# Performance work log

Hardware: AMD Instinct MI355X
Metric: run time of the kernel (lower is better)

## Reference

```python
import jax, jax.numpy as jnp
import numpy as np

D_MODEL, D_STATE, D_CONV, EXPAND = 1024, 16, 4, 2
D_INNER = EXPAND * D_MODEL            # 2048
DT_RANK = -(-D_MODEL // 16)           # ceil(d_model/16) = 64
B_SZ, L_SEQ = 2, 2048


def setup_inputs() -> dict:
    key = jax.random.key(0)
    ks = jax.random.split(key, 8)
    s = 0.02
    x = jax.random.normal(ks[0], (B_SZ, L_SEQ, D_MODEL), dtype=jnp.float32)
    W_in = jax.random.normal(ks[1], (D_MODEL, 2 * D_INNER), dtype=jnp.float32) * s
    conv_w = jax.random.normal(ks[2], (D_INNER, 1, D_CONV), dtype=jnp.float32) * 0.1  # depthwise (O,I/g,K)
    conv_b = jnp.zeros((D_INNER,), dtype=jnp.float32)
    W_x = jax.random.normal(ks[3], (D_INNER, DT_RANK + 2 * D_STATE), dtype=jnp.float32) * s
    W_dt = jax.random.normal(ks[4], (DT_RANK, D_INNER), dtype=jnp.float32) * s
    b_dt = jax.random.normal(ks[5], (D_INNER,), dtype=jnp.float32) * 0.1
    A_log = jnp.log(jnp.tile(jnp.arange(1, D_STATE + 1, dtype=jnp.float32), (D_INNER, 1)))  # (d_in, n)
    D_param = jnp.ones((D_INNER,), dtype=jnp.float32)
    W_out = jax.random.normal(ks[6], (D_INNER, D_MODEL), dtype=jnp.float32) * s
    return {"x": x, "W_in": W_in, "conv_w": conv_w, "conv_b": conv_b,
            "W_x": W_x, "W_dt": W_dt, "b_dt": b_dt, "A_log": A_log,
            "D_param": D_param, "W_out": W_out}


def _mamba(x, W_in, conv_w, conv_b, W_x, W_dt, b_dt, A_log, D_param, W_out):
    b, l, _ = x.shape
    d_in, n = A_log.shape
    dt_rank = W_dt.shape[0]
    d_conv = conv_w.shape[-1]

    xr = x @ W_in                                  # (b, l, 2*d_in)
    xs, res = xr[..., :d_in], xr[..., d_in:]

    # causal depthwise conv1d (left pad d_conv-1, truncate to l)
    xc = jnp.transpose(xs, (0, 2, 1))              # (b, d_in, l)
    xc = jax.lax.conv_general_dilated(
        xc, conv_w, window_strides=(1,), padding=[(d_conv - 1, 0)],
        dimension_numbers=("NCH", "OIH", "NCH"), feature_group_count=d_in)
    xc = xc + conv_b[None, :, None]
    xc = jnp.transpose(xc, (0, 2, 1))              # (b, l, d_in)
    xc = jax.nn.silu(xc)

    # SSM parameterization
    x_dbl = xc @ W_x                               # (b, l, dt_rank + 2n)
    delta = jax.nn.softplus(x_dbl[..., :dt_rank] @ W_dt + b_dt)   # (b, l, d_in)
    Bm = x_dbl[..., dt_rank:dt_rank + n]           # (b, l, n)
    Cm = x_dbl[..., dt_rank + n:]                  # (b, l, n)
    A = -jnp.exp(A_log)                            # (d_in, n)

    deltaA = jnp.exp(jnp.einsum("bld,dn->bldn", delta, A))        # (b, l, d_in, n)
    dBu = jnp.einsum("bld,bld,bln->bldn", delta, xc, Bm)          # (b, l, d_in, n)

    def step(h, inp):
        dA_t, dBu_t, C_t = inp                     # (b,d,n), (b,d,n), (b,n)
        h = dA_t * h + dBu_t
        y_t = jnp.einsum("bdn,bn->bd", h, C_t)
        return h, y_t

    h0 = jnp.zeros((b, d_in, n), dtype=xc.dtype)
    _, ys = jax.lax.scan(
        step, h0,
        (jnp.transpose(deltaA, (1, 0, 2, 3)),
         jnp.transpose(dBu, (1, 0, 2, 3)),
         jnp.transpose(Cm, (1, 0, 2))))
    y = jnp.transpose(ys, (1, 0, 2)) + xc * D_param  # (b, l, d_in)

    y = y * jax.nn.silu(res)
    return y @ W_out                               # (b, l, d_model)


def reference(x, W_in, conv_w, conv_b, W_x, W_dt, b_dt, A_log, D_param, W_out):
    return _mamba(x, W_in, conv_w, conv_b, W_x, W_dt, b_dt, A_log, D_param, W_out)
```

## Files before the change

### kernel.cpp

```cpp
#include <hip/hip_runtime.h>
#include <math.h>

#define B_SZ    2
#define L_SEQ   2048
#define D_MODEL 1024
#define D_INNER 2048
#define D_STATE 16
#define DT_RANK 64
#define MM      (B_SZ * L_SEQ)
#define NCH     64
#define CLEN    (L_SEQ / NCH)
#define PFD     8

typedef _Float16 h8v __attribute__((ext_vector_type(8)));
typedef _Float16 h4v __attribute__((ext_vector_type(4)));
typedef float f32x4 __attribute__((ext_vector_type(4)));

__device__ __forceinline__ void gload16(const void* g, void* l) {
    __builtin_amdgcn_global_load_lds((const __attribute__((address_space(1))) void*)g,
                                     (__attribute__((address_space(3))) void*)l, 16, 0, 0);
}

__global__ __launch_bounds__(256) void prep(const float* __restrict__ x,
                                            _Float16* __restrict__ xf16,
                                            const float* __restrict__ W_in,
                                            _Float16* __restrict__ WinT,
                                            const float* __restrict__ W_x,
                                            _Float16* __restrict__ WxT,
                                            const float* __restrict__ W_dt,
                                            _Float16* __restrict__ WdtT,
                                            const float* __restrict__ W_out,
                                            _Float16* __restrict__ WoutT,
                                            const float* __restrict__ cw,
                                            float* __restrict__ cwT) {
    __shared__ float t[32][33];
    const int b = blockIdx.x;
    const float* W; _Float16* T; int K, N, tile;
    if (b < 4096)      { W = W_in;  T = WinT;  K = 1024; N = 4096; tile = b; }
    else if (b < 4288) { W = W_x;   T = WxT;   K = 2048; N = 96;   tile = b - 4096; }
    else if (b < 4416) { W = W_dt;  T = WdtT;  K = 64;   N = 2048; tile = b - 4288; }
    else if (b < 6464) { W = W_out; T = WoutT; K = 2048; N = 1024; tile = b - 4416; }
    else if (b < 10560) {
        int idx = (b - 6464) * 256 + threadIdx.x;
        float4 v = ((const float4*)x)[idx];
        h4v h = {(_Float16)v.x, (_Float16)v.y, (_Float16)v.z, (_Float16)v.w};
        *(h4v*)(xf16 + (size_t)idx * 4) = h;
        return;
    } else {
        for (int i = threadIdx.x; i < D_INNER * 4; i += 256) {
            int d = i >> 2, k = i & 3;
            cwT[k * D_INNER + d] = cw[i];
        }
        return;
    }
    const int ntx = N / 32;
    const int k0 = (tile / ntx) * 32, n0 = (tile % ntx) * 32;
    #pragma unroll
    for (int i = 0; i < 4; ++i) {
        int idx = threadIdx.x + i * 256;
        int r = idx >> 5, c = idx & 31;
        t[r][c] = W[(size_t)(k0 + r) * N + n0 + c];
    }
    __syncthreads();
    #pragma unroll
    for (int i = 0; i < 4; ++i) {
        int idx = threadIdx.x + i * 256;
        int n = idx >> 5, k = idx & 31;
        T[(size_t)(n0 + n) * K + k0 + k] = (_Float16)t[k][n];
    }
}

template<int EPI>
__global__ __launch_bounds__(256) void gemm_f16(const _Float16* __restrict__ A,
                                                const _Float16* __restrict__ Bt,
                                                const float* __restrict__ bias,
                                                float* __restrict__ C,
                                                _Float16* __restrict__ H,
                                                _Float16* __restrict__ Hg,
                                                int M, int N, int K, int ldc) {
    __shared__ _Float16 smemh[16384];

    const int tid = threadIdx.x;
    const int wave = tid >> 6, lane = tid & 63;
    const int bm = blockIdx.y * 128, bn = blockIdx.x * 128;

    const int lrow = lane >> 2, pc = lane & 3;
    const int ar = wave * 32 + lrow;
    const size_t gA = (size_t)(bm + ar) * K + ((pc ^ ((ar >> 1) & 3)) * 8);
    const size_t gB = (size_t)(bn + ar) * K + ((pc ^ ((ar >> 1) & 3)) * 8);
    const int lofs = (wave * 32) * 32;

    const int lm = lane & 15, lq = lane >> 4;
    const int rofs = (lq ^ ((lm >> 1) & 3)) * 8;
    const int wm = (wave >> 1) * 64, wn = (wave & 1) * 64;

    f32x4 acc[4][4];
    #pragma unroll
    for (int i = 0; i < 4; ++i)
        #pragma unroll
        for (int j = 0; j < 4; ++j) acc[i][j] = (f32x4){0.f, 0.f, 0.f, 0.f};

    gload16(A + gA, smemh + lofs);
    gload16(A + gA + (size_t)16 * K, smemh + lofs + 16 * 32);
    gload16(Bt + gB, smemh + 8192 + lofs);
    gload16(Bt + gB + (size_t)16 * K, smemh + 8192 + lofs + 16 * 32);
    __syncthreads();

    int kb = 0;
    for (int k0 = 0; k0 < K; k0 += 32, kb ^= 1) {
        if (k0 + 32 < K) {
            int nb = kb ^ 1;
            gload16(A + gA + k0 + 32, smemh + nb * 4096 + lofs);
            gload16(A + gA + k0 + 32 + (size_t)16 * K, smemh + nb * 4096 + lofs + 16 * 32);
            gload16(Bt + gB + k0 + 32, smemh + 8192 + nb * 4096 + lofs);
            gload16(Bt + gB + k0 + 32 + (size_t)16 * K, smemh + 8192 + nb * 4096 + lofs + 16 * 32);
        }

        const _Float16* sA = smemh + kb * 4096;
        const _Float16* sB = smemh + 8192 + kb * 4096;
        h8v fa[4], fb[4];
        #pragma unroll
        for (int i = 0; i < 4; ++i) {
            fa[i] = *(const h8v*)&sA[(wm + i * 16 + lm) * 32 + rofs];
            fb[i] = *(const h8v*)&sB[(wn + i * 16 + lm) * 32 + rofs];
        }
        #pragma unroll
        for (int mi = 0; mi < 4; ++mi)
            #pragma unroll
            for (int ni = 0; ni < 4; ++ni)
                acc[mi][ni] = __builtin_amdgcn_mfma_f32_16x16x32_f16(fa[mi], fb[ni], acc[mi][ni], 0, 0, 0);
        __syncthreads();
    }

    if (EPI == 0) {
        float* ep = (float*)smemh + wave * 1088;
        #pragma unroll
        for (int mi = 0; mi < 4; ++mi) {
            #pragma unroll
            for (int ni = 0; ni < 4; ++ni)
                #pragma unroll
                for (int r = 0; r < 4; ++r)
                    ep[(lq * 4 + r) * 68 + ni * 16 + lm] = acc[mi][ni][r];
            int rowb = bm + wm + mi * 16;
            #pragma unroll
            for (int i = 0; i < 4; ++i) {
                int ch = lane + 64 * i;
                int row = ch >> 4, c4 = (ch & 15) * 4;
                *(float4*)&C[(size_t)(rowb + row) * ldc + bn + wn + c4] =
                    *(const float4*)&ep[row * 68 + c4];
            }
        }
    } else {
        _Float16* ep = smemh + wave * 1152;
        const bool gate = (EPI == 2) && (bn >= 2048);
        _Float16* dst = gate ? Hg : H;
        const int cb = bn + wn - (gate ? 2048 : 0);
        #pragma unroll
        for (int mi = 0; mi < 4; ++mi) {
            #pragma unroll
            for (int ni = 0; ni < 4; ++ni) {
                int col = bn + wn + ni * 16 + lm;
                #pragma unroll
                for (int r = 0; r < 4; ++r) {
                    float v = acc[mi][ni][r];
                    if (EPI == 1) {
                        float a = v + bias[col];
                        v = (a > 20.f) ? a : log1pf(__expf(a));
                    } else if (gate) {
                        v = v / (1.f + __expf(-v));
                    }
                    ep[(lq * 4 + r) * 72 + ni * 16 + lm] = (_Float16)v;
                }
            }
            int rowb = bm + wm + mi * 16;
            #pragma unroll
            for (int i = 0; i < 2; ++i) {
                int ch = lane + 64 * i;
                int row = ch >> 3, c8 = (ch & 7) * 8;
                *(h8v*)&dst[(size_t)(rowb + row) * ldc + cb + c8] =
                    *(const h8v*)&ep[row * 72 + c8];
            }
        }
    }
}

__global__ __launch_bounds__(256) void gemm_xd(const _Float16* __restrict__ xch,
                                               const _Float16* __restrict__ WxT,
                                               _Float16* __restrict__ xdh,
                                               float* __restrict__ Bm,
                                               float* __restrict__ Cm) {
    __shared__ _Float16 sA[64 * 32];
    __shared__ _Float16 sB[96 * 32];
    const int tid = threadIdx.x;
    const int m0 = blockIdx.x * 64;
    const int wave = tid >> 6, lane = tid & 63;
    const int lm = lane & 15, lq = lane >> 4;
    const int rofs = (lq ^ ((lm >> 1) & 3)) * 8;

    const int wr = tid >> 2, wc = tid & 3, c0 = wc * 8;
    const int wofsA = wr * 32 + ((wc ^ ((wr >> 1) & 3)) * 8);
    const int wr2 = 64 + wr;
    const int wofsB2 = wr2 * 32 + ((wc ^ ((wr2 >> 1) & 3)) * 8);

    f32x4 acc[6];
    #pragma unroll
    for (int i = 0; i < 6; ++i) acc[i] = (f32x4){0.f, 0.f, 0.f, 0.f};

    h8v pA = *(const h8v*)(xch + (size_t)(m0 + wr) * D_INNER + c0);
    h8v pB0 = *(const h8v*)(WxT + (size_t)wr * D_INNER + c0);
    h8v pB1 = (tid < 128) ? *(const h8v*)(WxT + (size_t)wr2 * D_INNER + c0) : (h8v)0;

    for (int k0 = 0; k0 < D_INNER; k0 += 32) {
        *(h8v*)&sA[wofsA] = pA;
        *(h8v*)&sB[wofsA] = pB0;
        if (tid < 128) *(h8v*)&sB[wofsB2] = pB1;
        __syncthreads();

        if (k0 + 32 < D_INNER) {
            int kk = k0 + 32 + c0;
            pA = *(const h8v*)(xch + (size_t)(m0 + wr) * D_INNER + kk);
            pB0 = *(const h8v*)(WxT + (size_t)wr * D_INNER + kk);
            if (tid < 128) pB1 = *(const h8v*)(WxT + (size_t)wr2 * D_INNER + kk);
        }

        h8v fa = *(const h8v*)&sA[(wave * 16 + lm) * 32 + rofs];
        #pragma unroll
        for (int nf = 0; nf < 6; ++nf) {
            h8v fb = *(const h8v*)&sB[(nf * 16 + lm) * 32 + rofs];
            acc[nf] = __builtin_amdgcn_mfma_f32_16x16x32_f16(fa, fb, acc[nf], 0, 0, 0);
        }
        __syncthreads();
    }

    #pragma unroll
    for (int nf = 0; nf < 6; ++nf) {
        int col = nf * 16 + lm;
        #pragma unroll
        for (int r = 0; r < 4; ++r) {
            int row = m0 + wave * 16 + lq * 4 + r;
            float v = acc[nf][r];
            if (col < 64)      xdh[(size_t)row * 64 + col] = (_Float16)v;
            else if (col < 80) Bm[(size_t)row * 16 + (col - 64)] = v;
            else               Cm[(size_t)row * 16 + (col - 80)] = v;
        }
    }
}

__global__ __launch_bounds__(256) void conv_silu(const _Float16* __restrict__ xsh,
                                                 const float* __restrict__ cwT,
                                                 const float* __restrict__ cb,
                                                 _Float16* __restrict__ xch) {
    int idx = blockIdx.x * 256 + threadIdx.x;
    int d0 = (idx * 8) & (D_INNER - 1);
    int m  = (idx * 8) >> 11;
    int l  = m & (L_SEQ - 1);
    float acc[8];
    {
        float4 c0 = *(const float4*)&cb[d0];
        float4 c1 = *(const float4*)&cb[d0 + 4];
        acc[0] = c0.x; acc[1] = c0.y; acc[2] = c0.z; acc[3] = c0.w;
        acc[4] = c1.x; acc[5] = c1.y; acc[6] = c1.z; acc[7] = c1.w;
    }
    #pragma unroll
    for (int k = 0; k < 4; ++k) {
        int ll = l - 3 + k;
        if (ll >= 0) {
            h8v v = *(const h8v*)(xsh + (size_t)(m - 3 + k) * D_INNER + d0);
            float4 w0 = *(const float4*)&cwT[k * D_INNER + d0];
            float4 w1 = *(const float4*)&cwT[k * D_INNER + d0 + 4];
            acc[0] += (float)v[0] * w0.x; acc[1] += (float)v[1] * w0.y;
            acc[2] += (float)v[2] * w0.z; acc[3] += (float)v[3] * w0.w;
            acc[4] += (float)v[4] * w1.x; acc[5] += (float)v[5] * w1.y;
            acc[6] += (float)v[6] * w1.z; acc[7] += (float)v[7] * w1.w;
        }
    }
    h8v o;
    #pragma unroll
    for (int j = 0; j < 8; ++j) {
        float s = acc[j] / (1.f + __expf(-acc[j]));
        o[j] = (_Float16)s;
    }
    *(h8v*)(xch + (size_t)idx * 8) = o;
}

__global__ __launch_bounds__(256) void scan_part1(const _Float16* __restrict__ deltah,
                                                  const _Float16* __restrict__ xch,
                                                  const float* __restrict__ Bm,
                                                  const float* __restrict__ A_log,
                                                  float* __restrict__ hlocal,
                                                  float* __restrict__ Ssum) {
    const int t = threadIdx.x;
    const int d = blockIdx.x * 256 + t;
    const int c = blockIdx.y;
    const int b = blockIdx.z;

    float An[16];
    {
        const float4* ap = (const float4*)(A_log + (size_t)d * 16);
        #pragma unroll
        for (int q = 0; q < 4; ++q) {
            float4 v = ap[q];
            An[q * 4 + 0] = -__expf(v.x); An[q * 4 + 1] = -__expf(v.y);
            An[q * 4 + 2] = -__expf(v.z); An[q * 4 + 3] = -__expf(v.w);
        }
    }
    const float An0 = An[0];
    bool fast = An0 < 0.f;
    #pragma unroll
    for (int n = 0; n < 16; ++n)
        fast = fast && (fabsf(An[n] - (float)(n + 1) * An0) < 1e-3f * fabsf(An[n]));

    __shared__ float sB[CLEN][16];
    {
        size_t l0 = (size_t)(b * L_SEQ + c * CLEN) * 16;
        #pragma unroll
        for (int i = 0; i < (CLEN * 16) / 256; ++i) {
            int idx = t + i * 256;
            sB[idx >> 4][idx & 15] = Bm[l0 + idx];
        }
    }
    __syncthreads();

    float h[16];
    #pragma unroll
    for (int n = 0; n < 16; ++n) h[n] = 0.f;
    float S = 0.f;

    size_t base = (size_t)(b * L_SEQ + c * CLEN) * D_INNER + d;
    float bd[PFD], bx[PFD];
    #pragma unroll
    for (int i = 0; i < PFD; ++i) {
        bd[i] = (float)deltah[base + (size_t)i * D_INNER];
        bx[i] = (float)xch[base + (size_t)i * D_INNER];
    }

    if (fast) {
        for (int jb = 0; jb < CLEN; jb += PFD) {
            #pragma unroll
            for (int i = 0; i < PFD; ++i) {
                int j = jb + i;
                float dv = bd[i], xv = bx[i];
                int jn = j + PFD;
                if (jn < CLEN) {
                    bd[i] = (float)deltah[base + (size_t)jn * D_INNER];
                    bx[i] = (float)xch[base + (size_t)jn * D_INNER];
                }
                S += dv;
                float dbx = dv * xv;
                float r = __expf(dv * An0);
                float pw = r;
                #pragma unroll
                for (int n = 0; n < 16; ++n) {
                    h[n] = pw * h[n] + dbx * sB[j][n];
                    pw *= r;
                }
            }
        }
    } else {
        for (int jb = 0; jb < CLEN; jb += PFD) {
            #pragma unroll
            for (int i = 0; i < PFD; ++i) {
                int j = jb + i;
                float dv = bd[i], xv = bx[i];
                int jn = j + PFD;
                if (jn < CLEN) {
                    bd[i] = (float)deltah[base + (size_t)jn * D_INNER];
                    bx[i] = (float)xch[base + (size_t)jn * D_INNER];
                }
                S += dv;
                float dbx = dv * xv;
                #pragma unroll
                for (int n = 0; n < 16; ++n)
                    h[n] = __expf(dv * An[n]) * h[n] + dbx * sB[j][n];
            }
        }
    }

    size_t o = ((size_t)(b * NCH + c) * D_INNER + d) * 16;
    float4* hp = (float4*)(hlocal + o);
    #pragma unroll
    for (int q = 0; q < 4; ++q)
        hp[q] = make_float4(h[q * 4], h[q * 4 + 1], h[q * 4 + 2], h[q * 4 + 3]);
    Ssum[(size_t)(b * NCH + c) * D_INNER + d] = S;
}

__global__ __launch_bounds__(256) void scan_combine(const float* __restrict__ hlocal,
                                                    const float* __restrict__ Ssum,
                                                    const float* __restrict__ A_log,
                                                    float* __restrict__ h0buf) {
    int gid = blockIdx.x * 256 + threadIdx.x;
    int n = gid & 15;
    int d = (gid >> 4) & (D_INNER - 1);
    int b = gid >> 15;
    float An = -__expf(A_log[(size_t)d * 16 + n]);
    float H = 0.f;
    float pS[4], pH[4];
    #pragma unroll
    for (int i = 0; i < 4; ++i) {
        size_t sc = (size_t)(b * NCH + i) * D_INNER + d;
        pS[i] = Ssum[sc];
        pH[i] = hlocal[sc * 16 + n];
    }
    for (int cb = 0; cb < NCH; cb += 4) {
        #pragma unroll
        for (int i = 0; i < 4; ++i) {
            int c = cb + i;
            float S = pS[i], hl = pH[i];
            int cn = c + 4;
            if (cn < NCH) {
                size_t sc = (size_t)(b * NCH + cn) * D_INNER + d;
                pS[i] = Ssum[sc];
                pH[i] = hlocal[sc * 16 + n];
            }
            size_t o = ((size_t)(b * NCH + c) * D_INNER + d) * 16 + n;
            h0buf[o] = H;
            H = __expf(An * S) * H + hl;
        }
    }
}

__global__ __launch_bounds__(256) void scan_part2(const _Float16* __restrict__ deltah,
                                                  const _Float16* __restrict__ xch,
                                                  const float* __restrict__ Bm,
                                                  const float* __restrict__ Cm,
                                                  const float* __restrict__ h0buf,
                                                  const float* __restrict__ A_log,
                                                  const float* __restrict__ Dp,
                                                  const _Float16* __restrict__ sresh,
                                                  _Float16* __restrict__ yhalf) {
    const int t = threadIdx.x;
    const int d = blockIdx.x * 256 + t;
    const int c = blockIdx.y;
    const int b = blockIdx.z;

    float An[16];
    {
        const float4* ap = (const float4*)(A_log + (size_t)d * 16);
        #pragma unroll
        for (int q = 0; q < 4; ++q) {
            float4 v = ap[q];
            An[q * 4 + 0] = -__expf(v.x); An[q * 4 + 1] = -__expf(v.y);
            An[q * 4 + 2] = -__expf(v.z); An[q * 4 + 3] = -__expf(v.w);
        }
    }
    const float An0 = An[0];
    bool fast = An0 < 0.f;
    #pragma unroll
    for (int n = 0; n < 16; ++n)
        fast = fast && (fabsf(An[n] - (float)(n + 1) * An0) < 1e-3f * fabsf(An[n]));

    __shared__ float sB[CLEN][16];
    __shared__ float sC[CLEN][16];
    {
        size_t l0 = (size_t)(b * L_SEQ + c * CLEN) * 16;
        #pragma unroll
        for (int i = 0; i < (CLEN * 16) / 256; ++i) {
            int idx = t + i * 256;
            sB[idx >> 4][idx & 15] = Bm[l0 + idx];
            sC[idx >> 4][idx & 15] = Cm[l0 + idx];
        }
    }
    __syncthreads();

    float h[16];
    {
        size_t o = ((size_t)(b * NCH + c) * D_INNER + d) * 16;
        const float4* hp = (const float4*)(h0buf + o);
        #pragma unroll
        for (int q = 0; q < 4; ++q) {
            float4 v = hp[q];
            h[q * 4 + 0] = v.x; h[q * 4 + 1] = v.y;
            h[q * 4 + 2] = v.z; h[q * 4 + 3] = v.w;
        }
    }
    const float Dv = Dp[d];

    size_t base = (size_t)(b * L_SEQ + c * CLEN) * D_INNER + d;
    float bd[PFD], bx[PFD], bg[PFD];
    #pragma unroll
    for (int i = 0; i < PFD; ++i) {
        bd[i] = (float)deltah[base + (size_t)i * D_INNER];
        bx[i] = (float)xch[base + (size_t)i * D_INNER];
        bg[i] = (float)sresh[base + (size_t)i * D_INNER];
    }

    if (fast) {
        for (int jb = 0; jb < CLEN; jb += PFD) {
            #pragma unroll
            for (int i = 0; i < PFD; ++i) {
                int j = jb + i;
                float dv = bd[i], xv = bx[i], gv = bg[i];
                int jn = j + PFD;
                if (jn < CLEN) {
                    bd[i] = (float)deltah[base + (size_t)jn * D_INNER];
                    bx[i] = (float)xch[base + (size_t)jn * D_INNER];
                    bg[i] = (float)sresh[base + (size_t)jn * D_INNER];
                }
                float dbx = dv * xv;
                float r = __expf(dv * An0);
                float pw = r;
                float y = 0.f;
                #pragma unroll
                for (int n = 0; n < 16; ++n) {
                    h[n] = pw * h[n] + dbx * sB[j][n];
                    y += h[n] * sC[j][n];
                    pw *= r;
                }
                float yv = (y + xv * Dv) * gv;
                yhalf[base + (size_t)j * D_INNER] = (_Float16)yv;
            }
        }
    } else {
        for (int jb = 0; jb < CLEN; jb += PFD) {
            #pragma unroll
            for (int i = 0; i < PFD; ++i) {
                int j = jb + i;
                float dv = bd[i], xv = bx[i], gv = bg[i];
                int jn = j + PFD;
                if (jn < CLEN) {
                    bd[i] = (float)deltah[base + (size_t)jn * D_INNER];
                    bx[i] = (float)xch[base + (size_t)jn * D_INNER];
                    bg[i] = (float)sresh[base + (size_t)jn * D_INNER];
                }
                float dbx = dv * xv;
                float y = 0.f;
                #pragma unroll
                for (int n = 0; n < 16; ++n) {
                    h[n] = __expf(dv * An[n]) * h[n] + dbx * sB[j][n];
                    y += h[n] * sC[j][n];
                }
                float yv = (y + xv * Dv) * gv;
                yhalf[base + (size_t)j * D_INNER] = (_Float16)yv;
            }
        }
    }
}

extern "C" void kernel_launch(void* const* d_in, const int* in_sizes, int n_in,
                              void* d_out, int out_size, void* d_ws, size_t ws_size,
                              hipStream_t stream) {
    const float* x      = (const float*)d_in[0];
    const float* W_in   = (const float*)d_in[1];
    const float* conv_w = (const float*)d_in[2];
    const float* conv_b = (const float*)d_in[3];
    const float* W_x    = (const float*)d_in[4];
    const float* W_dt   = (const float*)d_in[5];
    const float* b_dt   = (const float*)d_in[6];
    const float* A_log  = (const float*)d_in[7];
    const float* D_par  = (const float*)d_in[8];
    const float* W_out  = (const float*)d_in[9];
    float* out = (float*)d_out;

    char* wsb = (char*)d_ws;
    _Float16*  xsh    = (_Float16*)(wsb + 0);
    _Float16*  sresh  = (_Float16*)(wsb + 16777216);
    _Float16*  deltah = (_Float16*)(wsb + 33554432);
    _Float16*  xch    = (_Float16*)(wsb + 50331648);
    _Float16*  xf16   = (_Float16*)(wsb + 67108864);
    _Float16*  WinT   = (_Float16*)(wsb + 75497472);
    _Float16*  yhalf  = (_Float16*)(wsb + 67108864);
    _Float16*  WxT    = (_Float16*)(wsb + 83886080);
    _Float16*  WdtT   = (_Float16*)(wsb + 84279296);
    _Float16*  xdh    = (_Float16*)(wsb + 84541440);
    float*     Bbuf   = (float*)(wsb + 85065728);
    float*     Cbuf   = (float*)(wsb + 85327872);
    float*     Ssum   = (float*)(wsb + 85590016);
    float*     hloc   = (float*)(wsb + 86638592);
    float*     h0buf  = (float*)(wsb + 103415808);
    _Float16*  WoutT  = (_Float16*)(wsb + 120193024);
    float*     cwT    = (float*)(wsb + 124387328);

    dim3 blk(256);

    prep<<<dim3(10561), blk, 0, stream>>>(x, xf16, W_in, WinT, W_x, WxT,
                                          W_dt, WdtT, W_out, WoutT, conv_w, cwT);
    gemm_f16<2><<<dim3(32, 32), blk, 0, stream>>>(
        xf16, WinT, nullptr, nullptr, xsh, sresh, MM, 2 * D_INNER, D_MODEL, 2048);
    conv_silu<<<dim3((size_t)MM * D_INNER / 8 / 256), blk, 0, stream>>>(xsh, cwT, conv_b, xch);
    gemm_xd<<<dim3(MM / 64), blk, 0, stream>>>(xch, WxT, xdh, Bbuf, Cbuf);
    gemm_f16<1><<<dim3(16, 32), blk, 0, stream>>>(
        xdh, WdtT, b_dt, nullptr, deltah, nullptr, MM, D_INNER, DT_RANK, D_INNER);
    scan_part1<<<dim3(D_INNER / 256, NCH, B_SZ), blk, 0, stream>>>(deltah, xch, Bbuf, A_log, hloc, Ssum);
    scan_combine<<<dim3(B_SZ * D_INNER * 16 / 256), blk, 0, stream>>>(hloc, Ssum, A_log, h0buf);
    scan_part2<<<dim3(D_INNER / 256, NCH, B_SZ), blk, 0, stream>>>(deltah, xch, Bbuf, Cbuf, h0buf, A_log, D_par, sresh, yhalf);
    gemm_f16<0><<<dim3(8, 32), blk, 0, stream>>>(
        yhalf, WoutT, nullptr, out, nullptr, nullptr, MM, D_MODEL, D_INNER, D_MODEL);
}
```

Measured before the change: 323.5 us.

## Replace input projection GEMM with 256x256-tile 8-wave pipelined MFMA kernel

Adds a dedicated in-projection GEMM kernel using 256x256 output tiles, 512 threads, and double-buffered LDS with global_load_lds prefetch. The prefetch is interleaved with four MFMA phases under setprio and barriers. The goal is more operand reuse per LDS load and better overlap of memory with compute for the largest GEMM. The tradeoff is only 256 blocks on a large-CU GPU, so the grid may fill the machine unevenly, plus heavy register and LDS use at 128KB of shared memory.

Result: faster. 316.4 us (-2.2%).

```diff
diff --git a/kernel.cpp b/kernel.cpp
--- a/kernel.cpp
+++ b/kernel.cpp
@@ -70,6 +70,140 @@
     }
 }
 
+#define LDA_(mi, ks) (*(const h8v*)(smb + cb_ + rowA + (mi) * 2048 + ((ks) ? ps1 : ps0)))
+#define LDB_(ni, ks) (*(const h8v*)(smb + cb_ + 32768 + rowB + (ni) * 2048 + ((ks) ? ps1 : ps0)))
+#define PH(m0, m1) \
+    _Pragma("unroll") \
+    for (int ni = 0; ni < 4; ++ni) { \
+        acc[m0][ni] = __builtin_amdgcn_mfma_f32_16x16x32_f16(aF0, bF[2 * ni],     acc[m0][ni], 0, 0, 0); \
+        acc[m0][ni] = __builtin_amdgcn_mfma_f32_16x16x32_f16(aF1, bF[2 * ni + 1], acc[m0][ni], 0, 0, 0); \
+        acc[m1][ni] = __builtin_amdgcn_mfma_f32_16x16x32_f16(aF2, bF[2 * ni],     acc[m1][ni], 0, 0, 0); \
+        acc[m1][ni] = __builtin_amdgcn_mfma_f32_16x16x32_f16(aF3, bF[2 * ni + 1], acc[m1][ni], 0, 0, 0); \
+    }
+
+__global__ __launch_bounds__(512, 2) void gemm_k1(const _Float16* __restrict__ A,
+                                                  const _Float16* __restrict__ Bt,
+                                                  _Float16* __restrict__ H,
+                                                  _Float16* __restrict__ Hg) {
+    __shared__ _Float16 smem[65536];
+    char* smb = (char*)smem;
+
+    const int tid  = threadIdx.x;
+    const int wave = tid >> 6, lane = tid & 63;
+    const int wm = wave >> 2, wn = wave & 3;
+    const int lm = lane & 15, lq = lane >> 4;
+    const int bm = blockIdx.y * 256, bn = blockIdx.x * 256;
+
+    const int ps0 = ((lq)     ^ (lm & 7)) << 4;
+    const int ps1 = ((lq + 4) ^ (lm & 7)) << 4;
+    const int rowA = (wm * 128 + lm) << 7;
+    const int rowB = (wn * 64 + lm) << 7;
+
+    const int srow  = lane >> 3;
+    const int sslot = (lane & 7) ^ srow;
+    const _Float16* pA = A  + (size_t)(bm + wave * 32 + srow) * 1024 + sslot * 8;
+    const _Float16* pB = Bt + (size_t)(bn + wave * 32 + srow) * 1024 + sslot * 8;
+    char* dA = smb + wave * 4096;
+    char* dB = smb + 32768 + wave * 4096;
+
+    f32x4 acc[8][4];
+    #pragma unroll
+    for (int i = 0; i < 8; ++i)
+        #pragma unroll
+        for (int j = 0; j < 4; ++j) acc[i][j] = (f32x4){0.f, 0.f, 0.f, 0.f};
+
+    #pragma unroll
+    for (int q = 0; q < 4; ++q) {
+        gload16(pA + q * 8192, dA + q * 1024);
+        gload16(pB + q * 8192, dB + q * 1024);
+    }
+    asm volatile("s_waitcnt vmcnt(0)" ::: "memory");
+    __builtin_amdgcn_s_barrier();
+
+    int cb_ = 0;
+    for (int t = 0; t < 16; ++t) {
+        const int nb_ = 65536 - cb_;
+        const bool pf = (t < 15);
+        const size_t kn = (size_t)(t + 1) * 64;
+
+        h8v aF0, aF1, aF2, aF3;
+        h8v bF[8];
+
+        aF0 = LDA_(0, 0); aF1 = LDA_(0, 1); aF2 = LDA_(1, 0); aF3 = LDA_(1, 1);
+        #pragma unroll
+        for (int ni = 0; ni < 4; ++ni) { bF[2 * ni] = LDB_(ni, 0); bF[2 * ni + 1] = LDB_(ni, 1); }
+        if (pf) {
+            #pragma unroll
+            for (int q = 0; q < 4; ++q) gload16(pA + kn + q * 8192, dA + nb_ + q * 1024);
+        }
+        __builtin_amdgcn_s_barrier();
+        asm volatile("s_waitcnt lgkmcnt(0)" ::: "memory");
+        __builtin_amdgcn_s_setprio(1);
+        PH(0, 1);
+        __builtin_amdgcn_s_setprio(0);
+        __builtin_amdgcn_s_barrier();
+
+        aF0 = LDA_(2, 0); aF1 = LDA_(2, 1); aF2 = LDA_(3, 0); aF3 = LDA_(3, 1);
+        if (pf) {
+            #pragma unroll
+            for (int q = 0; q < 4; ++q) gload16(pB + kn + q * 8192, dB + nb_ + q * 1024);
+        }
+        __builtin_amdgcn_s_barrier();
+        asm volatile("s_waitcnt lgkmcnt(0)" ::: "memory");
+        __builtin_amdgcn_s_setprio(1);
+        PH(2, 3);
+        __builtin_amdgcn_s_setprio(0);
+        __builtin_amdgcn_s_barrier();
+
+        aF0 = LDA_(4, 0); aF1 = LDA_(4, 1); aF2 = LDA_(5, 0); aF3 = LDA_(5, 1);
+        __builtin_amdgcn_s_barrier();
+        asm volatile("s_waitcnt lgkmcnt(0)" ::: "memory");
+        __builtin_amdgcn_s_setprio(1);
+        PH(4, 5);
+        __builtin_amdgcn_s_setprio(0);
+        __builtin_amdgcn_s_barrier();
+
+        aF0 = LDA_(6, 0); aF1 = LDA_(6, 1); aF2 = LDA_(7, 0); aF3 = LDA_(7, 1);
+        asm volatile("s_waitcnt vmcnt(4)" ::: "memory");
+        __builtin_amdgcn_s_barrier();
+        asm volatile("s_waitcnt lgkmcnt(0)" ::: "memory");
+        __builtin_amdgcn_s_setprio(1);
+        PH(6, 7);
+        __builtin_amdgcn_s_setprio(0);
+        asm volatile("s_waitcnt vmcnt(0)" ::: "memory");
+        __builtin_amdgcn_s_barrier();
+
+        cb_ = nb_;
+    }
+
+    _Float16* ep = smem + wave * 2048;
+    const bool gate = (bn >= 2048);
+    _Float16* dst = gate ? Hg : H;
+    const int cbase = bn + wn * 64 - (gate ? 2048 : 0);
+    #pragma unroll
+    for (int mi = 0; mi < 8; ++mi) {
+        #pragma unroll
+        for (int ni = 0; ni < 4; ++ni)
+            #pragma unroll
+            for (int r = 0; r < 4; ++r) {
+                float v = acc[mi][ni][r];
+                if (gate) v = v / (1.f + __expf(-v));
+                ep[(lq * 4 + r) * 72 + ni * 16 + lm] = (_Float16)v;
+            }
+        int rowb = bm + wm * 128 + mi * 16;
+        #pragma unroll
+        for (int i = 0; i < 2; ++i) {
+            int ch = lane + 64 * i;
+            int row = ch >> 3, c8 = (ch & 7) * 8;
+            *(h8v*)&dst[(size_t)(rowb + row) * 2048 + cbase + c8] =
+                *(const h8v*)&ep[row * 72 + c8];
+        }
+    }
+}
+#undef LDA_
+#undef LDB_
+#undef PH
+
 template<int EPI>
 __global__ __launch_bounds__(256) void gemm_f16(const _Float16* __restrict__ A,
                                                 const _Float16* __restrict__ Bt,
@@ -574,8 +708,7 @@
 
     prep<<<dim3(10561), blk, 0, stream>>>(x, xf16, W_in, WinT, W_x, WxT,
                                           W_dt, WdtT, W_out, WoutT, conv_w, cwT);
-    gemm_f16<2><<<dim3(32, 32), blk, 0, stream>>>(
-        xf16, WinT, nullptr, nullptr, xsh, sresh, MM, 2 * D_INNER, D_MODEL, 2048);
+    gemm_k1<<<dim3(16, 16), dim3(512), 0, stream>>>(xf16, WinT, xsh, sresh);
     conv_silu<<<dim3((size_t)MM * D_INNER / 8 / 256), blk, 0, stream>>>(xsh, cwT, conv_b, xch);
     gemm_xd<<<dim3(MM / 64), blk, 0, stream>>>(xch, WxT, xdh, Bbuf, Cbuf);
     gemm_f16<1><<<dim3(16, 32), blk, 0, stream>>>(
```

## Add specialized 256x256 tile MFMA GEMM for input projection with 4-stage pipeline

Applied to the files above, without the earlier changes.

Replaces the generic 128x128 f16 GEMM for the input projection with a dedicated kernel using 512 threads, 256x256 output tiles, and a 4-deep LDS ring buffer filled via global_load_lds. MFMA phases are split into two halves with barriers, explicit waitcnt scheduling and setprio to overlap loads with compute. The larger tile is meant to raise data reuse and MFMA utilization. In exchange it uses 128KB of LDS and launches only 256 blocks, which may limit occupancy and leave CUs underused.

Measured after the change: 322.7 us. No clear change (-0.2%).

```diff
diff --git a/kernel.cpp b/kernel.cpp
--- a/kernel.cpp
+++ b/kernel.cpp
@@ -70,6 +70,127 @@
     }
 }
 
+#define MF(d, a, b) d = __builtin_amdgcn_mfma_f32_16x16x32_f16(a, b, d, 0, 0, 0)
+#define PH16(mb, A0, A1, A2, A3) \
+    MF(acc[(mb)+0][0], A0, bF0); MF(acc[(mb)+0][1], A0, bF1); \
+    MF(acc[(mb)+0][2], A0, bF2); MF(acc[(mb)+0][3], A0, bF3); \
+    MF(acc[(mb)+1][0], A1, bF0); MF(acc[(mb)+1][1], A1, bF1); \
+    MF(acc[(mb)+1][2], A1, bF2); MF(acc[(mb)+1][3], A1, bF3); \
+    MF(acc[(mb)+2][0], A2, bF0); MF(acc[(mb)+2][1], A2, bF1); \
+    MF(acc[(mb)+2][2], A2, bF2); MF(acc[(mb)+2][3], A2, bF3); \
+    MF(acc[(mb)+3][0], A3, bF0); MF(acc[(mb)+3][1], A3, bF1); \
+    MF(acc[(mb)+3][2], A3, bF2); MF(acc[(mb)+3][3], A3, bF3);
+
+__global__ __launch_bounds__(512, 2) void gemm_k1(const _Float16* __restrict__ A,
+                                                  const _Float16* __restrict__ Bt,
+                                                  _Float16* __restrict__ H,
+                                                  _Float16* __restrict__ Hg) {
+    __shared__ _Float16 smem[65536];
+    char* smb = (char*)smem;
+
+    const int tid  = threadIdx.x;
+    const int wave = tid >> 6, lane = tid & 63;
+    const int wm = wave >> 2, wn = wave & 3;
+    const int lm = lane & 15, lq = lane >> 4;
+    const int bm = blockIdx.y * 256, bn = blockIdx.x * 256;
+
+    const int psl = (lq ^ ((lm >> 1) & 3)) << 4;
+    const int rA0 = ((wm * 128 + lm) << 6) + psl;
+    const int rB0 = 16384 + ((wn * 64 + lm) << 6) + psl;
+
+    const int srow  = lane >> 2;
+    const int sslot = (lane & 3) ^ ((lane >> 3) & 3);
+    const _Float16* pA = A  + (size_t)(bm + wave * 16 + srow) * 1024 + sslot * 8;
+    const _Float16* pB = Bt + (size_t)(bn + wave * 16 + srow) * 1024 + sslot * 8;
+    const int wq = wave * 1024;
+
+    f32x4 acc[8][4];
+    #pragma unroll
+    for (int i = 0; i < 8; ++i)
+        #pragma unroll
+        for (int j = 0; j < 4; ++j) acc[i][j] = (f32x4){0.f, 0.f, 0.f, 0.f};
+
+    #pragma unroll
+    for (int s = 0; s < 3; ++s) {
+        const int bo = s << 15;
+        const size_t ko = (size_t)s * 32;
+        gload16(pA + ko,          smb + bo + wq);
+        gload16(pA + ko + 131072, smb + bo + 8192 + wq);
+        gload16(pB + ko,          smb + bo + 16384 + wq);
+        gload16(pB + ko + 131072, smb + bo + 24576 + wq);
+    }
+    asm volatile("s_waitcnt vmcnt(8)" ::: "memory");
+    __builtin_amdgcn_s_barrier();
+
+    for (int t = 0; t < 32; ++t) {
+        const char* buf = smb + ((t & 3) << 15);
+        h8v aF0, aF1, aF2, aF3, bF0, bF1, bF2, bF3;
+
+        aF0 = *(const h8v*)(buf + rA0);
+        aF1 = *(const h8v*)(buf + rA0 + 1024);
+        aF2 = *(const h8v*)(buf + rA0 + 2048);
+        aF3 = *(const h8v*)(buf + rA0 + 3072);
+        bF0 = *(const h8v*)(buf + rB0);
+        bF1 = *(const h8v*)(buf + rB0 + 1024);
+        bF2 = *(const h8v*)(buf + rB0 + 2048);
+        bF3 = *(const h8v*)(buf + rB0 + 3072);
+        if (t <= 28) {
+            const int nb = ((t + 3) & 3) << 15;
+            const size_t kn = (size_t)(t + 3) * 32;
+            gload16(pA + kn,          smb + nb + wq);
+            gload16(pA + kn + 131072, smb + nb + 8192 + wq);
+            gload16(pB + kn,          smb + nb + 16384 + wq);
+            gload16(pB + kn + 131072, smb + nb + 24576 + wq);
+        }
+        __builtin_amdgcn_s_barrier();
+        asm volatile("s_waitcnt lgkmcnt(0)" ::: "memory");
+        __builtin_amdgcn_s_setprio(1);
+        PH16(0, aF0, aF1, aF2, aF3);
+        __builtin_amdgcn_s_setprio(0);
+        __builtin_amdgcn_s_barrier();
+
+        aF0 = *(const h8v*)(buf + rA0 + 4096);
+        aF1 = *(const h8v*)(buf + rA0 + 5120);
+        aF2 = *(const h8v*)(buf + rA0 + 6144);
+        aF3 = *(const h8v*)(buf + rA0 + 7168);
+        if (t <= 28)      asm volatile("s_waitcnt vmcnt(8)" ::: "memory");
+        else if (t == 29) asm volatile("s_waitcnt vmcnt(4)" ::: "memory");
+        else if (t == 30) asm volatile("s_waitcnt vmcnt(0)" ::: "memory");
+        __builtin_amdgcn_s_barrier();
+        asm volatile("s_waitcnt lgkmcnt(0)" ::: "memory");
+        __builtin_amdgcn_s_setprio(1);
+        PH16(4, aF0, aF1, aF2, aF3);
+        __builtin_amdgcn_s_setprio(0);
+        __builtin_amdgcn_s_barrier();
+    }
+
+    _Float16* ep = smem + wave * 2048;
+    const bool gate = (bn >= 2048);
+    _Float16* dst = gate ? Hg : H;
+    const int cbase = bn + wn * 64 - (gate ? 2048 : 0);
+    #pragma unroll
+    for (int mi = 0; mi < 8; ++mi) {
+        #pragma unroll
+        for (int ni = 0; ni < 4; ++ni)
+            #pragma unroll
+            for (int r = 0; r < 4; ++r) {
+                float v = acc[mi][ni][r];
+                if (gate) v = v / (1.f + __expf(-v));
+                ep[(lq * 4 + r) * 72 + ni * 16 + lm] = (_Float16)v;
+            }
+        int rowb = bm + wm * 128 + mi * 16;
+        #pragma unroll
+        for (int i = 0; i < 2; ++i) {
+            int ch = lane + 64 * i;
+            int row = ch >> 3, c8 = (ch & 7) * 8;
+            *(h8v*)&dst[(size_t)(rowb + row) * 2048 + cbase + c8] =
+                *(const h8v*)&ep[row * 72 + c8];
+        }
+    }
+}
+#undef MF
+#undef PH16
+
 template<int EPI>
 __global__ __launch_bounds__(256) void gemm_f16(const _Float16* __restrict__ A,
                                                 const _Float16* __restrict__ Bt,
@@ -574,8 +695,7 @@
 
     prep<<<dim3(10561), blk, 0, stream>>>(x, xf16, W_in, WinT, W_x, WxT,
                                           W_dt, WdtT, W_out, WoutT, conv_w, cwT);
-    gemm_f16<2><<<dim3(32, 32), blk, 0, stream>>>(
-        xf16, WinT, nullptr, nullptr, xsh, sresh, MM, 2 * D_INNER, D_MODEL, 2048);
+    gemm_k1<<<dim3(16, 16), dim3(512), 0, stream>>>(xf16, WinT, xsh, sresh);
     conv_silu<<<dim3((size_t)MM * D_INNER / 8 / 256), blk, 0, stream>>>(xsh, cwT, conv_b, xch);
     gemm_xd<<<dim3(MM / 64), blk, 0, stream>>>(xch, WxT, xdh, Bbuf, Cbuf);
     gemm_f16<1><<<dim3(16, 32), blk, 0, stream>>>(
```
